# Kernel tuning notes

Hardware: AMD Instinct MI355X
Metric: run time of the kernel (lower is better)

## Reference

```python
import jax, jax.numpy as jnp
import numpy as np

B, IN, H, OUT = 4096, 1024, 2048, 1024
EPS = 1e-5  # added to std (not variance), matching the torch module


def _ln(z, a, b):
    # torch.std default is unbiased (ddof=1); eps added to sigma
    mu = jnp.mean(z, axis=1, keepdims=True)
    sigma = jnp.std(z, axis=1, ddof=1, keepdims=True)
    return (z - mu) / (sigma + EPS) * a + b


def setup_inputs() -> dict:
    key = jax.random.key(0)
    ks = iter(jax.random.split(key, 40))
    W = lambda i, o: (jax.random.normal(next(ks), (o, i), jnp.float32) / np.sqrt(i)).astype(jnp.float32)
    bz = lambda o: jnp.zeros((o,), jnp.float32)
    d = {
        "inp": jax.random.normal(next(ks), (B, IN), jnp.float32),
        "h_0": jax.random.normal(next(ks), (B, H), jnp.float32),
        "c_0": jax.random.normal(next(ks), (B, H), jnp.float32),
        # h-side gate linears (H -> H)
        "Wfh": W(H, H), "bfh": bz(H), "Wih": W(H, H), "bih": bz(H),
        "Wch": W(H, H), "bch": bz(H), "Woh": W(H, H), "boh": bz(H),
        # x-side gate linears (IN -> H)
        "Wfx": W(IN, H), "bfx": bz(H), "Wix": W(IN, H), "bix": bz(H),
        "Wcx": W(IN, H), "bcx": bz(H), "Wox": W(IN, H), "box": bz(H),
        # decoder (H -> OUT)
        "Wdec": W(H, OUT), "bdec": bz(OUT),
        # LayerNormalization params (a2 ones, b2 zeros), shape (1, H)
        "ax": jnp.ones((1, H), jnp.float32), "bx": jnp.zeros((1, H), jnp.float32),
        "ah": jnp.ones((1, H), jnp.float32), "bh": jnp.zeros((1, H), jnp.float32),
        "ac": jnp.ones((1, H), jnp.float32), "bc": jnp.zeros((1, H), jnp.float32),
    }
    return d


def reference(inp, h_0, c_0,
              Wfh, bfh, Wih, bih, Wch, bch, Woh, boh,
              Wfx, bfx, Wix, bix, Wcx, bcx, Wox, box,
              Wdec, bdec, ax, bx, ah, bh, ac, bc):
    lin = lambda x, W, b: x @ W.T + b
    gate = lambda wx, bx_, wh, bh_: (_ln(lin(inp, wx, bx_), ax, bx)
                                     + _ln(lin(h_0, wh, bh_), ah, bh))
    f_g = jax.nn.sigmoid(gate(Wfx, bfx, Wfh, bfh))
    i_g = jax.nn.sigmoid(gate(Wix, bix, Wih, bih))
    c_tilda = jnp.tanh(gate(Wcx, bcx, Wch, bch))
    cx = f_g * c_0 + i_g * c_tilda
    o_g = jax.nn.sigmoid(gate(Wox, box, Woh, boh))
    hx = o_g * jnp.tanh(_ln(cx, ac, bc))
    out = lin(hx, Wdec, bdec)  # decoder applied to hidden state (vectorized over batch)
    return (out, hx, cx)
```

## Files before the change

kernel.cpp:

```cpp
#include <hip/hip_runtime.h>

#define NB   4096
#define NIN  1024
#define NH   2048
#define NOUT 1024
#define NH4  8192

typedef short short8 __attribute__((ext_vector_type(8)));
typedef float f32x4 __attribute__((ext_vector_type(4)));
typedef float f32x16 __attribute__((ext_vector_type(16)));
typedef unsigned short ushort8v __attribute__((ext_vector_type(8)));

__device__ __forceinline__ float bf2f(unsigned short u) {
  union { unsigned int i; float f; } c; c.i = ((unsigned int)u) << 16; return c.f;
}
__device__ __forceinline__ unsigned short f2bf(float f) {
  union { float f; unsigned int i; } c; c.f = f;
  unsigned int u = c.i;
  u += 0x7FFFu + ((u >> 16) & 1u);
  return (unsigned short)(u >> 16);
}
__device__ __forceinline__ float sigf(float x) { return 1.0f / (1.0f + __expf(-x)); }
__device__ __forceinline__ float tanh_f(float x) { return 1.0f - 2.0f / (__expf(2.0f * x) + 1.0f); }

#define CNT_INP  ((size_t)NB * NIN)
#define CNT_H0   ((size_t)NB * NH)
#define CNT_WXG  ((size_t)NH * NIN)
#define CNT_WHG  ((size_t)NH * NH)
#define CNT_WD   ((size_t)NOUT * NH)
#define OFF_XB   ((size_t)0)
#define OFF_H0B  (OFF_XB + CNT_INP)
#define OFF_HXB  (OFF_H0B + CNT_H0)
#define OFF_WX   (OFF_HXB + CNT_H0)
#define OFF_WH   (OFF_WX + 4 * CNT_WXG)
#define OFF_WD   (OFF_WH + 4 * CNT_WHG)
#define OFF_ZX   (OFF_WD + CNT_WD)
#define OFF_ZH   (OFF_ZX + (size_t)NB * NH4)
#define CVT_TOTAL (OFF_WD + CNT_WD)

struct CvtArgs { const float* src[11]; };

__global__ __launch_bounds__(256) void cvt_all(CvtArgs a, unsigned short* __restrict__ dstBase) {
  const size_t i = ((size_t)blockIdx.x * 256 + threadIdx.x) * 8;
  if (i >= CVT_TOTAL) return;
  const size_t cnt[11] = {CNT_INP, CNT_H0, CNT_WXG, CNT_WXG, CNT_WXG, CNT_WXG,
                          CNT_WHG, CNT_WHG, CNT_WHG, CNT_WHG, CNT_WD};
  const size_t dst[11] = {OFF_XB, OFF_H0B,
                          OFF_WX, OFF_WX + CNT_WXG, OFF_WX + 2 * CNT_WXG, OFF_WX + 3 * CNT_WXG,
                          OFF_WH, OFF_WH + CNT_WHG, OFF_WH + 2 * CNT_WHG, OFF_WH + 3 * CNT_WHG,
                          OFF_WD};
  size_t base = 0;
#pragma unroll
  for (int s = 0; s < 11; s++) {
    if (i < base + cnt[s]) {
      const size_t off = i - base;
      const float* sp = a.src[s] + off;
      float4 v0 = *(const float4*)(sp);
      float4 v1 = *(const float4*)(sp + 4);
      ushort8v o;
      o[0] = f2bf(v0.x); o[1] = f2bf(v0.y); o[2] = f2bf(v0.z); o[3] = f2bf(v0.w);
      o[4] = f2bf(v1.x); o[5] = f2bf(v1.y); o[6] = f2bf(v1.z); o[7] = f2bf(v1.w);
      *(ushort8v*)(dstBase + dst[s] + off) = o;
      return;
    }
    base += cnt[s];
  }
}

__device__ __forceinline__ void gload16(const void* g, void* l) {
  __builtin_amdgcn_global_load_lds((const __attribute__((address_space(1))) void*)g,
                                   (__attribute__((address_space(3))) void*)l, 16, 0, 0);
}

template<int MT, bool BOUT>
__device__ __forceinline__ void gemm_core32(const unsigned short* __restrict__ A,
                                            const unsigned short* __restrict__ Bm,
                                            const float* b0p, const float* b1p,
                                            const float* b2p, const float* b3p,
                                            float* __restrict__ Cf, unsigned short* __restrict__ Cb,
                                            int N, int K) {
  constexpr int TM = MT * 64;
  __shared__ __align__(16) unsigned short As[TM * 64];
  __shared__ __align__(16) unsigned short Bs[128 * 64];
  const int t = threadIdx.x;
  const int w = t >> 6;
  const int lane = t & 63;
  const int r31 = lane & 31;
  const int hi = lane >> 5;
  const int rloc = lane >> 3;
  const int slot = lane & 7;
  const int m0 = blockIdx.y * TM;
  const int n0 = blockIdx.x * 128;
  const int wm = (w >> 1) * (MT * 32);
  const int wn = (w & 1) * 64;

  f32x16 acc[MT][2];
#pragma unroll
  for (int i = 0; i < MT; i++)
#pragma unroll
    for (int j = 0; j < 2; j++)
#pragma unroll
      for (int r = 0; r < 16; r++) acc[i][j][r] = 0.f;

  const unsigned short* AgP[2 * MT];
  unsigned short* AsP[2 * MT];
#pragma unroll
  for (int q = 0; q < 2 * MT; q++) {
    const int iss = w + 4 * q;
    const int bblk = slot ^ rloc ^ (iss & 3);
    AgP[q] = A + (size_t)(m0 + iss * 8 + rloc) * K + bblk * 8;
    AsP[q] = As + iss * 512;
  }
  const unsigned short* BgP[4];
  unsigned short* BsP[4];
#pragma unroll
  for (int q = 0; q < 4; q++) {
    const int iss = w + 4 * q;
    const int bblk = slot ^ rloc ^ (iss & 3);
    BgP[q] = Bm + (size_t)(n0 + iss * 8 + rloc) * K + bblk * 8;
    BsP[q] = Bs + iss * 512;
  }

  const int swz = (r31 & 7) ^ ((r31 >> 3) & 3);

  for (int k0 = 0; k0 < K; k0 += 64) {
#pragma unroll
    for (int q = 0; q < 2 * MT; q++) gload16(AgP[q] + k0, AsP[q]);
#pragma unroll
    for (int q = 0; q < 4; q++) gload16(BgP[q] + k0, BsP[q]);
    __syncthreads();

#pragma unroll
    for (int ks = 0; ks < 4; ks++) {
      const int phys = ((ks * 2 + hi) ^ swz) * 8;
      short8 af[MT], bf[2];
#pragma unroll
      for (int mt = 0; mt < MT; mt++) af[mt] = *(const short8*)&As[(wm + mt * 32 + r31) * 64 + phys];
#pragma unroll
      for (int jt = 0; jt < 2; jt++) bf[jt] = *(const short8*)&Bs[(wn + jt * 32 + r31) * 64 + phys];
#pragma unroll
      for (int mt = 0; mt < MT; mt++)
#pragma unroll
        for (int jt = 0; jt < 2; jt++)
          acc[mt][jt] = __builtin_amdgcn_mfma_f32_32x32x16_bf16(af[mt], bf[jt], acc[mt][jt], 0, 0, 0);
    }
    __syncthreads();
  }

#pragma unroll
  for (int mt = 0; mt < MT; mt++) {
#pragma unroll
    for (int jt = 0; jt < 2; jt++) {
      const int col = n0 + wn + jt * 32 + r31;
      const float* bp = (col < 2048) ? b0p : ((col < 4096) ? b1p : ((col < 6144) ? b2p : b3p));
      const float bv = bp[col & 2047];
      const int rowb = m0 + wm + mt * 32 + hi * 4;
#pragma unroll
      for (int reg = 0; reg < 16; reg++) {
        const int row = rowb + (reg & 3) + 8 * (reg >> 2);
        const float v = acc[mt][jt][reg] + bv;
        const size_t idx = (size_t)row * N + col;
        if (BOUT) Cb[idx] = f2bf(v);
        else      Cf[idx] = v;
      }
    }
  }
}

__global__ __launch_bounds__(256) void gemm_dual(const unsigned short* __restrict__ Xb,
                                                 const unsigned short* __restrict__ Wx,
                                                 const unsigned short* __restrict__ H0b,
                                                 const unsigned short* __restrict__ Wh,
                                                 const float* bx0, const float* bx1,
                                                 const float* bx2, const float* bx3,
                                                 const float* bh0, const float* bh1,
                                                 const float* bh2, const float* bh3,
                                                 unsigned short* __restrict__ Zx,
                                                 unsigned short* __restrict__ Zh) {
  if (blockIdx.z == 0)
    gemm_core32<2, true>(Xb, Wx, bx0, bx1, bx2, bx3, nullptr, Zx, NH4, NIN);
  else
    gemm_core32<2, true>(H0b, Wh, bh0, bh1, bh2, bh3, nullptr, Zh, NH4, NH);
}

__global__ __launch_bounds__(256) void gemm_dec(const unsigned short* __restrict__ HXb,
                                                const unsigned short* __restrict__ Wd,
                                                const float* __restrict__ bdec,
                                                float* __restrict__ out) {
  gemm_core32<1, false>(HXb, Wd, bdec, bdec, bdec, bdec, out, nullptr, NOUT, NH);
}

__global__ __launch_bounds__(256) void ln_gates(const unsigned short* __restrict__ Zx,
                                                const unsigned short* __restrict__ Zh,
                                                const float* __restrict__ c0,
                                                const float* __restrict__ ax, const float* __restrict__ bx,
                                                const float* __restrict__ ah, const float* __restrict__ bh,
                                                const float* __restrict__ ac, const float* __restrict__ bc,
                                                float* __restrict__ out_top,
                                                unsigned short* __restrict__ hx_bf) {
  const int b = blockIdx.x;
  const int t = threadIdx.x;
  const int n = t * 8;
  const int w = t >> 6;
  const int lane = t & 63;
  const float inv_n = 1.0f / 2048.0f, inv_nm1 = 1.0f / 2047.0f;

  short8 zx[4], zh[4];
  const size_t rowoff = (size_t)b * NH4;
#pragma unroll
  for (int g = 0; g < 4; g++) {
    zx[g] = *(const short8*)(Zx + rowoff + g * NH + n);
    zh[g] = *(const short8*)(Zh + rowoff + g * NH + n);
  }

  float s[16];
#pragma unroll
  for (int g = 0; g < 4; g++) {
    float su = 0, sq = 0, su2 = 0, sq2 = 0;
#pragma unroll
    for (int j = 0; j < 8; j++) {
      float v = bf2f((unsigned short)zx[g][j]); su += v; sq += v * v;
      float u = bf2f((unsigned short)zh[g][j]); su2 += u; sq2 += u * u;
    }
    s[g * 4 + 0] = su; s[g * 4 + 1] = sq; s[g * 4 + 2] = su2; s[g * 4 + 3] = sq2;
  }
#pragma unroll
  for (int i = 0; i < 16; i++) {
    float v = s[i];
#pragma unroll
    for (int o = 32; o > 0; o >>= 1) v += __shfl_xor(v, o, 64);
    s[i] = v;
  }
  __shared__ float red[4][16];
  __shared__ float red2[4][2];
  if (lane == 0) {
#pragma unroll
    for (int i = 0; i < 16; i++) red[w][i] = s[i];
  }
  __syncthreads();
#pragma unroll
  for (int i = 0; i < 16; i++) s[i] = red[0][i] + red[1][i] + red[2][i] + red[3][i];

  float mux[4], ivx[4], muh[4], ivh[4];
#pragma unroll
  for (int g = 0; g < 4; g++) {
    mux[g] = s[g * 4 + 0] * inv_n;
    float vx = fmaxf((s[g * 4 + 1] - s[g * 4 + 0] * mux[g]) * inv_nm1, 0.0f);
    ivx[g] = 1.0f / (sqrtf(vx) + 1e-5f);
    muh[g] = s[g * 4 + 2] * inv_n;
    float vh = fmaxf((s[g * 4 + 3] - s[g * 4 + 2] * muh[g]) * inv_nm1, 0.0f);
    ivh[g] = 1.0f / (sqrtf(vh) + 1e-5f);
  }

  float axl[8], bxl[8], ahl[8], bhl[8], c0l[8];
  *(float4*)&axl[0] = *(const float4*)(ax + n); *(float4*)&axl[4] = *(const float4*)(ax + n + 4);
  *(float4*)&bxl[0] = *(const float4*)(bx + n); *(float4*)&bxl[4] = *(const float4*)(bx + n + 4);
  *(float4*)&ahl[0] = *(const float4*)(ah + n); *(float4*)&ahl[4] = *(const float4*)(ah + n + 4);
  *(float4*)&bhl[0] = *(const float4*)(bh + n); *(float4*)&bhl[4] = *(const float4*)(bh + n + 4);
  const float* c0p = c0 + (size_t)b * NH + n;
  *(float4*)&c0l[0] = *(const float4*)(c0p); *(float4*)&c0l[4] = *(const float4*)(c0p + 4);

  float cx[8], og[8];
  float cs = 0, css = 0;
#pragma unroll
  for (int j = 0; j < 8; j++) {
    float pre[4];
#pragma unroll
    for (int g = 0; g < 4; g++) {
      float vx = bf2f((unsigned short)zx[g][j]);
      float vh = bf2f((unsigned short)zh[g][j]);
      pre[g] = ((vx - mux[g]) * ivx[g]) * axl[j] + bxl[j]
             + ((vh - muh[g]) * ivh[g]) * ahl[j] + bhl[j];
    }
    float fg = sigf(pre[0]);
    float ig = sigf(pre[1]);
    float ct = tanh_f(pre[2]);
    og[j] = sigf(pre[3]);
    float c = fg * c0l[j] + ig * ct;
    cx[j] = c; cs += c; css += c * c;
  }
#pragma unroll
  for (int o = 32; o > 0; o >>= 1) { cs += __shfl_xor(cs, o, 64); css += __shfl_xor(css, o, 64); }
  if (lane == 0) { red2[w][0] = cs; red2[w][1] = css; }
  __syncthreads();
  cs = red2[0][0] + red2[1][0] + red2[2][0] + red2[3][0];
  css = red2[0][1] + red2[1][1] + red2[2][1] + red2[3][1];
  const float muc = cs * inv_n;
  const float varc = fmaxf((css - cs * muc) * inv_nm1, 0.0f);
  const float ivc = 1.0f / (sqrtf(varc) + 1e-5f);

  float acl[8], bcl[8];
  *(float4*)&acl[0] = *(const float4*)(ac + n); *(float4*)&acl[4] = *(const float4*)(ac + n + 4);
  *(float4*)&bcl[0] = *(const float4*)(bc + n); *(float4*)&bcl[4] = *(const float4*)(bc + n + 4);

  float hx[8];
#pragma unroll
  for (int j = 0; j < 8; j++)
    hx[j] = og[j] * tanh_f((cx[j] - muc) * ivc * acl[j] + bcl[j]);

  float* hx_out = out_top + (size_t)NB * NOUT + (size_t)b * NH + n;
  float* cx_out = out_top + (size_t)NB * NOUT + (size_t)NB * NH + (size_t)b * NH + n;
  float4 v;
  v.x = hx[0]; v.y = hx[1]; v.z = hx[2]; v.w = hx[3]; *(float4*)(hx_out) = v;
  v.x = hx[4]; v.y = hx[5]; v.z = hx[6]; v.w = hx[7]; *(float4*)(hx_out + 4) = v;
  v.x = cx[0]; v.y = cx[1]; v.z = cx[2]; v.w = cx[3]; *(float4*)(cx_out) = v;
  v.x = cx[4]; v.y = cx[5]; v.z = cx[6]; v.w = cx[7]; *(float4*)(cx_out + 4) = v;
  ushort8v hb;
#pragma unroll
  for (int j = 0; j < 8; j++) hb[j] = f2bf(hx[j]);
  *(ushort8v*)(hx_bf + (size_t)b * NH + n) = hb;
}

extern "C" void kernel_launch(void* const* d_in, const int* in_sizes, int n_in,
                              void* d_out, int out_size, void* d_ws, size_t ws_size,
                              hipStream_t stream) {
  const float* inp = (const float*)d_in[0];
  const float* h0  = (const float*)d_in[1];
  const float* c0  = (const float*)d_in[2];
  const float* bhg[4] = {(const float*)d_in[4], (const float*)d_in[6], (const float*)d_in[8], (const float*)d_in[10]};
  const float* bxg[4] = {(const float*)d_in[12], (const float*)d_in[14], (const float*)d_in[16], (const float*)d_in[18]};
  const float* bdec = (const float*)d_in[20];
  const float* ax = (const float*)d_in[21];
  const float* bx = (const float*)d_in[22];
  const float* ah = (const float*)d_in[23];
  const float* bh = (const float*)d_in[24];
  const float* ac = (const float*)d_in[25];
  const float* bc = (const float*)d_in[26];

  unsigned short* wsb = (unsigned short*)d_ws;
  unsigned short* Xb   = wsb + OFF_XB;
  unsigned short* H0b  = wsb + OFF_H0B;
  unsigned short* HXb  = wsb + OFF_HXB;
  unsigned short* Wx4b = wsb + OFF_WX;
  unsigned short* Wh4b = wsb + OFF_WH;
  unsigned short* Wdb  = wsb + OFF_WD;
  unsigned short* Zx   = wsb + OFF_ZX;
  unsigned short* Zh   = wsb + OFF_ZH;

  CvtArgs ca;
  ca.src[0] = inp; ca.src[1] = h0;
  ca.src[2] = (const float*)d_in[11]; ca.src[3] = (const float*)d_in[13];
  ca.src[4] = (const float*)d_in[15]; ca.src[5] = (const float*)d_in[17];
  ca.src[6] = (const float*)d_in[3];  ca.src[7] = (const float*)d_in[5];
  ca.src[8] = (const float*)d_in[7];  ca.src[9] = (const float*)d_in[9];
  ca.src[10] = (const float*)d_in[19];
  {
    const size_t nthr = CVT_TOTAL / 8;
    cvt_all<<<dim3((unsigned)((nthr + 255) / 256)), dim3(256), 0, stream>>>(ca, wsb);
  }

  gemm_dual<<<dim3(NH4 / 128, NB / 128, 2), 256, 0, stream>>>(
      Xb, Wx4b, H0b, Wh4b,
      bxg[0], bxg[1], bxg[2], bxg[3],
      bhg[0], bhg[1], bhg[2], bhg[3],
      Zx, Zh);

  ln_gates<<<dim3(NB), 256, 0, stream>>>(Zx, Zh, c0, ax, bx, ah, bh, ac, bc, (float*)d_out, HXb);

  gemm_dec<<<dim3(NOUT / 128, NB / 64), 256, 0, stream>>>(HXb, Wdb, bdec, (float*)d_out);
}
```

Measured before the change: 572.3 us.

## Replace dual gate GEMM with 256x256-tile 8-wave pipelined MFMA kernel

```diff
diff --git a/kernel.cpp b/kernel.cpp
--- a/kernel.cpp
+++ b/kernel.cpp
@@ -70,6 +70,168 @@
 __device__ __forceinline__ void gload16(const void* g, void* l) {
   __builtin_amdgcn_global_load_lds((const __attribute__((address_space(1))) void*)g,
                                    (__attribute__((address_space(3))) void*)l, 16, 0, 0);
+}
+
+#define SCH0  __builtin_amdgcn_sched_barrier(0)
+#define BARR  __builtin_amdgcn_s_barrier()
+#define LGKM0 asm volatile("s_waitcnt lgkmcnt(0)" ::: "memory")
+#define VMC6  asm volatile("s_waitcnt vmcnt(6)" ::: "memory")
+#define VMC0  asm volatile("s_waitcnt vmcnt(0)" ::: "memory")
+
+__global__ __launch_bounds__(512) void gemm_dual8(
+    const unsigned short* __restrict__ Xb, const unsigned short* __restrict__ Wx,
+    const unsigned short* __restrict__ H0b, const unsigned short* __restrict__ Wh,
+    const float* bx0, const float* bx1, const float* bx2, const float* bx3,
+    const float* bh0, const float* bh1, const float* bh2, const float* bh3,
+    unsigned short* __restrict__ Zx, unsigned short* __restrict__ Zh) {
+  __shared__ __align__(16) unsigned short As[2][256 * 64];
+  __shared__ __align__(16) unsigned short Bs[2][256 * 64];
+
+  const unsigned short* Ag; const unsigned short* Bg;
+  const float *p0, *p1, *p2, *p3; unsigned short* Cg; int K;
+  if (blockIdx.z == 0) { Ag = Xb;  Bg = Wx; Cg = Zx; K = NIN; p0 = bx0; p1 = bx1; p2 = bx2; p3 = bx3; }
+  else                 { Ag = H0b; Bg = Wh; Cg = Zh; K = NH;  p0 = bh0; p1 = bh1; p2 = bh2; p3 = bh3; }
+
+  const int t    = threadIdx.x;
+  const int wid  = t >> 6;
+  const int lane = t & 63;
+  const int m15  = lane & 15;
+  const int g4   = lane >> 4;
+  const int wm   = wid >> 2;
+  const int wn   = wid & 3;
+  const int rloc = lane >> 3;
+  const int slot = lane & 7;
+  const int ck   = slot ^ rloc ^ (wid & 3);
+  const int m0   = blockIdx.y * 256;
+  const int n0   = blockIdx.x * 256;
+  const int NT   = K >> 6;
+  const size_t thrOff = (size_t)(wid * 8 + rloc) * K + ck * 8;
+
+#define STAGE_HALF(G, R0, H, TT, LDBASE) do {                                                     \
+    const unsigned short* _gs = (G) + thrOff + (size_t)((R0) + (H) * 128) * K + (size_t)(TT) * 64; \
+    unsigned short* _ld = (LDBASE) + ((H) * 128 + wid * 8) * 64;                                   \
+    gload16(_gs, _ld);                                                                             \
+    gload16(_gs + (size_t)64 * K, _ld + 4096);                                                     \
+  } while (0)
+
+#define LD8(S, ROW, KC) (*(const short8*)&(S)[(ROW) * 64 + (((KC) ^ (((ROW) & 7) ^ (((ROW) >> 3) & 3))) * 8)])
+
+  f32x4 acc[8][4];
+#pragma unroll
+  for (int m = 0; m < 8; m++)
+#pragma unroll
+    for (int n = 0; n < 4; n++)
+#pragma unroll
+      for (int r = 0; r < 4; r++) acc[m][n][r] = 0.f;
+
+  STAGE_HALF(Ag, m0, 0, 0, As[0]);
+  STAGE_HALF(Ag, m0, 1, 0, As[0]);
+  STAGE_HALF(Bg, n0, 0, 0, Bs[0]);
+  STAGE_HALF(Bg, n0, 1, 0, Bs[0]);
+  STAGE_HALF(Bg, n0, 0, 1, Bs[1]);
+  STAGE_HALF(Bg, n0, 1, 1, Bs[1]);
+  STAGE_HALF(Ag, m0, 0, 1, As[1]);
+  VMC6;
+  SCH0; BARR; SCH0;
+
+  for (int kt = 0; kt < NT; ++kt) {
+    const int cur = kt & 1;
+    const unsigned short* sA = As[cur];
+    const unsigned short* sB = Bs[cur];
+    const int tp1 = (kt + 1 < NT) ? kt + 1 : NT - 1;
+    const int tp2 = (kt + 2 < NT) ? kt + 2 : NT - 1;
+    short8 b[4][2], a[4][2];
+
+#pragma unroll
+    for (int n = 0; n < 4; n++) {
+      const int row = wn * 64 + n * 16 + m15;
+      b[n][0] = LD8(sB, row, g4);
+      b[n][1] = LD8(sB, row, 4 + g4);
+    }
+#pragma unroll
+    for (int m = 0; m < 4; m++) {
+      const int row = wm * 128 + m * 16 + m15;
+      a[m][0] = LD8(sA, row, g4);
+      a[m][1] = LD8(sA, row, 4 + g4);
+    }
+    STAGE_HALF(Ag, m0, 1, tp1, As[cur ^ 1]);
+    SCH0; BARR; LGKM0; SCH0;
+    __builtin_amdgcn_s_setprio(1);
+#pragma unroll
+    for (int m = 0; m < 4; m++)
+#pragma unroll
+      for (int n = 0; n < 2; n++) {
+        acc[m][n] = __builtin_amdgcn_mfma_f32_16x16x32_bf16(a[m][0], b[n][0], acc[m][n], 0, 0, 0);
+        acc[m][n] = __builtin_amdgcn_mfma_f32_16x16x32_bf16(a[m][1], b[n][1], acc[m][n], 0, 0, 0);
+      }
+    __builtin_amdgcn_s_setprio(0);
+    SCH0; BARR; SCH0;
+
+    STAGE_HALF(Bg, n0, 0, tp2, Bs[cur]);
+    SCH0; BARR; LGKM0; SCH0;
+    __builtin_amdgcn_s_setprio(1);
+#pragma unroll
+    for (int m = 0; m < 4; m++)
+#pragma unroll
+      for (int n = 0; n < 2; n++) {
+        acc[m][2 + n] = __builtin_amdgcn_mfma_f32_16x16x32_bf16(a[m][0], b[2 + n][0], acc[m][2 + n], 0, 0, 0);
+        acc[m][2 + n] = __builtin_amdgcn_mfma_f32_16x16x32_bf16(a[m][1], b[2 + n][1], acc[m][2 + n], 0, 0, 0);
+      }
+    __builtin_amdgcn_s_setprio(0);
+    SCH0; BARR; SCH0;
+
+#pragma unroll
+    for (int m = 0; m < 4; m++) {
+      const int row = wm * 128 + 64 + m * 16 + m15;
+      a[m][0] = LD8(sA, row, g4);
+      a[m][1] = LD8(sA, row, 4 + g4);
+    }
+    STAGE_HALF(Bg, n0, 1, tp2, Bs[cur]);
+    SCH0; BARR; LGKM0; SCH0;
+    __builtin_amdgcn_s_setprio(1);
+#pragma unroll
+    for (int m = 0; m < 4; m++)
+#pragma unroll
+      for (int n = 0; n < 2; n++) {
+        acc[4 + m][n] = __builtin_amdgcn_mfma_f32_16x16x32_bf16(a[m][0], b[n][0], acc[4 + m][n], 0, 0, 0);
+        acc[4 + m][n] = __builtin_amdgcn_mfma_f32_16x16x32_bf16(a[m][1], b[n][1], acc[4 + m][n], 0, 0, 0);
+      }
+    __builtin_amdgcn_s_setprio(0);
+    SCH0; BARR; SCH0;
+
+    STAGE_HALF(Ag, m0, 0, tp2, As[cur]);
+    SCH0; BARR; SCH0;
+    __builtin_amdgcn_s_setprio(1);
+#pragma unroll
+    for (int m = 0; m < 4; m++)
+#pragma unroll
+      for (int n = 0; n < 2; n++) {
+        acc[4 + m][2 + n] = __builtin_amdgcn_mfma_f32_16x16x32_bf16(a[m][0], b[2 + n][0], acc[4 + m][2 + n], 0, 0, 0);
+        acc[4 + m][2 + n] = __builtin_amdgcn_mfma_f32_16x16x32_bf16(a[m][1], b[2 + n][1], acc[4 + m][2 + n], 0, 0, 0);
+      }
+    __builtin_amdgcn_s_setprio(0);
+    VMC6;
+    SCH0; BARR; SCH0;
+  }
+
+  VMC0;
+
+#pragma unroll
+  for (int n = 0; n < 4; n++) {
+    const int col = n0 + wn * 64 + n * 16 + m15;
+    const float* bp = (col < 2048) ? p0 : ((col < 4096) ? p1 : ((col < 6144) ? p2 : p3));
+    const float bv = bp[col & 2047];
+#pragma unroll
+    for (int m = 0; m < 8; m++) {
+      const int rowb = m0 + wm * 128 + m * 16 + g4 * 4;
+#pragma unroll
+      for (int r = 0; r < 4; r++) {
+        Cg[(size_t)(rowb + r) * NH4 + col] = f2bf(acc[m][n][r] + bv);
+      }
+    }
+  }
+#undef STAGE_HALF
+#undef LD8
 }
 
 template<int MT, bool BOUT>
@@ -167,22 +329,6 @@
   }
 }
 
-__global__ __launch_bounds__(256) void gemm_dual(const unsigned short* __restrict__ Xb,
-                                                 const unsigned short* __restrict__ Wx,
-                                                 const unsigned short* __restrict__ H0b,
-                                                 const unsigned short* __restrict__ Wh,
-                                                 const float* bx0, const float* bx1,
-                                                 const float* bx2, const float* bx3,
-                                                 const float* bh0, const float* bh1,
-                                                 const float* bh2, const float* bh3,
-                                                 unsigned short* __restrict__ Zx,
-                                                 unsigned short* __restrict__ Zh) {
-  if (blockIdx.z == 0)
-    gemm_core32<2, true>(Xb, Wx, bx0, bx1, bx2, bx3, nullptr, Zx, NH4, NIN);
-  else
-    gemm_core32<2, true>(H0b, Wh, bh0, bh1, bh2, bh3, nullptr, Zh, NH4, NH);
-}
-
 __global__ __launch_bounds__(256) void gemm_dec(const unsigned short* __restrict__ HXb,
                                                 const unsigned short* __restrict__ Wd,
                                                 const float* __restrict__ bdec,
@@ -349,7 +495,7 @@
     cvt_all<<<dim3((unsigned)((nthr + 255) / 256)), dim3(256), 0, stream>>>(ca, wsb);
   }
 
-  gemm_dual<<<dim3(NH4 / 128, NB / 128, 2), 256, 0, stream>>>(
+  gemm_dual8<<<dim3(NH4 / 256, NB / 256, 2), 512, 0, stream>>>(
       Xb, Wx4b, H0b, Wh4b,
       bxg[0], bxg[1], bxg[2], bxg[3],
       bhg[0], bhg[1], bhg[2], bhg[3],
```

Result: slower. 635.4 us (+11.0%).
